# Kernel optimization log

Hardware: AMD Instinct MI355X
Metric: run time of the kernel (lower is better)

The kernel has to match this reference:

```python
import jax, jax.numpy as jnp
import numpy as np

EMBED = 1024
HEADS = 16
HEAD_DIM = EMBED // HEADS
N, L = 8, 1024


def setup_inputs() -> dict:
    key = jax.random.key(0)
    ks = jax.random.split(key, 12)
    s = 1.0 / np.sqrt(EMBED)
    return {
        "values": jax.random.normal(ks[0], (N, L, EMBED), jnp.float32),
        "keys": jax.random.normal(ks[1], (N, L, EMBED), jnp.float32),
        "queries": jax.random.normal(ks[2], (N, L, EMBED), jnp.float32),
        "mask": jax.random.randint(ks[3], (N, 1, L, L), 0, 2, jnp.int32),
        "Wv": jax.random.normal(ks[4], (EMBED, EMBED), jnp.float32) * s,
        "bv": jnp.zeros((EMBED,), jnp.float32),
        "Wk": jax.random.normal(ks[5], (EMBED, EMBED), jnp.float32) * s,
        "bk": jnp.zeros((EMBED,), jnp.float32),
        "Wq": jax.random.normal(ks[6], (EMBED, EMBED), jnp.float32) * s,
        "bq": jnp.zeros((EMBED,), jnp.float32),
        "Wo": jax.random.normal(ks[7], (EMBED, EMBED), jnp.float32) * s,
        "bo": jnp.zeros((EMBED,), jnp.float32),
    }


def reference(values, keys, queries, mask, Wv, bv, Wk, bk, Wq, bq, Wo, bo):
    n, q_len = queries.shape[0], queries.shape[1]
    # Linear projections (torch Linear: x @ W.T + b)
    v = values @ Wv.T + bv
    k = keys @ Wk.T + bk
    q = queries @ Wq.T + bq
    # split heads: [N, L, H, D]
    v = v.reshape(n, -1, HEADS, HEAD_DIM)
    k = k.reshape(n, -1, HEADS, HEAD_DIM)
    q = q.reshape(n, q_len, HEADS, HEAD_DIM)
    # energy: [N, H, Q, K]
    energy = jnp.einsum("nqhd,nkhd->nhqk", q, k)
    energy = jnp.where(mask == 0, jnp.float32(-1e20), energy)
    attention = jax.nn.softmax(energy / jnp.sqrt(jnp.float32(EMBED)), axis=3)
    out = jnp.einsum("nhqk,nkhd->nqhd", attention, v).reshape(n, q_len, EMBED)
    return out @ Wo.T + bo
```

## Files before the change

### kernel.cpp

```cpp
#include <hip/hip_runtime.h>
#include <hip/hip_bf16.h>


typedef __attribute__((ext_vector_type(8))) short short8;
typedef __attribute__((ext_vector_type(8))) __bf16 bf16x8;
typedef __attribute__((ext_vector_type(4))) float f32x4;
typedef __attribute__((ext_vector_type(16))) float f32x16;
typedef __attribute__((ext_vector_type(4))) unsigned short ushort4v;

static __device__ __forceinline__ unsigned short f2bf(float x) {
  union { float f; unsigned u; } v; v.f = x;
  unsigned r = v.u + 0x7FFFu + ((v.u >> 16) & 1u);
  return (unsigned short)(r >> 16);
}

static __device__ __forceinline__ f32x4 mfma16(short8 a, short8 b, f32x4 c) {
  return __builtin_amdgcn_mfma_f32_16x16x32_bf16(
      __builtin_bit_cast(bf16x8, a), __builtin_bit_cast(bf16x8, b), c, 0, 0, 0);
}
static __device__ __forceinline__ f32x16 mfma32(short8 a, short8 b, f32x16 c) {
  return __builtin_amdgcn_mfma_f32_32x32x16_bf16(
      __builtin_bit_cast(bf16x8, a), __builtin_bit_cast(bf16x8, b), c, 0, 0, 0);
}

static __device__ __forceinline__ void gll16(const unsigned short* g, unsigned short* l) {
  __builtin_amdgcn_global_load_lds(
      (const __attribute__((address_space(1))) unsigned int*)(const void*)g,
      (__attribute__((address_space(3))) unsigned int*)(void*)l, 16, 0, 0);
}

static __device__ __forceinline__ unsigned cvtpk(float lo, float hi) {
  unsigned r;
  asm("v_cvt_pk_bf16_f32 %0, %1, %2" : "=v"(r) : "v"(lo), "v"(hi));
  return r;
}

__global__ __launch_bounds__(256)
void cvt_kernel(const float* __restrict__ in, unsigned short* __restrict__ out, int n8)
{
  int i = blockIdx.x * 256 + threadIdx.x;
  if (i >= n8) return;
  float4 a = ((const float4*)in)[i * 2];
  float4 b = ((const float4*)in)[i * 2 + 1];
  union { short8 v; unsigned short u[8]; } pk;
  pk.u[0] = f2bf(a.x); pk.u[1] = f2bf(a.y); pk.u[2] = f2bf(a.z); pk.u[3] = f2bf(a.w);
  pk.u[4] = f2bf(b.x); pk.u[5] = f2bf(b.y); pk.u[6] = f2bf(b.z); pk.u[7] = f2bf(b.w);
  ((short8*)out)[i] = pk.v;
}

__global__ __launch_bounds__(256)
void maskpack_kernel(const int* __restrict__ m, unsigned long long* __restrict__ M64)
{
  const int lane = threadIdx.x & 63, wid = threadIdx.x >> 6;
  const int wi = blockIdx.x * 4 + wid;
  unsigned long long b = __ballot(m[(size_t)wi * 64 + lane] != 0);
  if (lane == 0) M64[wi] = b;
}

template<int MODE>
__global__ __launch_bounds__(256)
void gemm_kernel(const unsigned short* __restrict__ A, const unsigned short* __restrict__ B,
                 const float* __restrict__ bias, void* __restrict__ outp)
{
  __shared__ alignas(16) unsigned short As[128][32];
  __shared__ alignas(16) unsigned short Bs[128][32];
  const int tid = threadIdx.x, lane = tid & 63, wid = tid >> 6;
  const int l15 = lane & 15, lg = lane >> 4;
  const int bm = blockIdx.x, bn = blockIdx.y;
  const int wr = (wid >> 1) * 64, wc = (wid & 1) * 64;

  f32x4 acc[4][4] = {};
  const int o = wid * 1024 + lane * 16;
  const unsigned short* gA0 = A + (size_t)(bm * 128 + (o >> 6)) * 1024 + ((o & 63) >> 1);
  const unsigned short* gA1 = gA0 + 64 * 1024;
  const unsigned short* gB0 = B + (size_t)(bn * 128 + (o >> 6)) * 1024 + ((o & 63) >> 1);
  const unsigned short* gB1 = gB0 + 64 * 1024;
  unsigned short* lA0 = &As[0][0] + wid * 512;
  unsigned short* lA1 = lA0 + 2048;
  unsigned short* lB0 = &Bs[0][0] + wid * 512;
  unsigned short* lB1 = lB0 + 2048;

  for (int k0 = 0; k0 < 1024; k0 += 32) {
    __syncthreads();
    gll16(gA0 + k0, lA0); gll16(gA1 + k0, lA1);
    gll16(gB0 + k0, lB0); gll16(gB1 + k0, lB1);
    __syncthreads();
    short8 af[4], bf[4];
#pragma unroll
    for (int f = 0; f < 4; ++f) {
      af[f] = *(const short8*)&As[wr + f * 16 + l15][lg * 8];
      bf[f] = *(const short8*)&Bs[wc + f * 16 + l15][lg * 8];
    }
#pragma unroll
    for (int r = 0; r < 4; ++r)
#pragma unroll
      for (int c = 0; c < 4; ++c)
        acc[r][c] = mfma16(af[r], bf[c], acc[r][c]);
  }

#pragma unroll
  for (int r = 0; r < 4; ++r) {
    const int mb = bm * 128 + wr + r * 16 + lg * 4;
#pragma unroll
    for (int c = 0; c < 4; ++c) {
      const int col = bn * 128 + wc + c * 16 + l15;
      const float bv = bias[col];
      if (MODE == 0) {
        unsigned short* O = (unsigned short*)outp;
#pragma unroll
        for (int i = 0; i < 4; ++i)
          O[(size_t)(mb + i) * 1024 + col] = f2bf(acc[r][c][i] + bv);
      } else if (MODE == 1) {
        unsigned short* O = (unsigned short*)outp;
        const int n = mb >> 10, l = mb & 1023, hh = col >> 6, d = col & 63;
        union { ushort4v v; unsigned short u[4]; } pk;
#pragma unroll
        for (int i = 0; i < 4; ++i) pk.u[i] = f2bf(acc[r][c][i] + bv);
        *(ushort4v*)&O[(size_t)((n * 16 + hh) * 64 + d) * 1024 + l] = pk.v;
      } else {
        float* O = (float*)outp;
#pragma unroll
        for (int i = 0; i < 4; ++i)
          O[(size_t)(mb + i) * 1024 + col] = acc[r][c][i] + bv;
      }
    }
  }
}

__global__ __launch_bounds__(256)
void attn_kernel(const unsigned short* __restrict__ Q,
                 const unsigned short* __restrict__ K,
                 const unsigned short* __restrict__ VT,
                 const unsigned long long* __restrict__ M64,
                 unsigned short* __restrict__ AO)
{
  __shared__ alignas(16) unsigned short Ks[2][4096];
  __shared__ alignas(16) unsigned short Vs[2][4096];
  const int tid = threadIdx.x, lane = tid & 63, wid = tid >> 6;
  const int l31 = lane & 31, hi4 = (lane >> 5) * 4;
  const int w = (blockIdx.x & 7) * 128 + (blockIdx.x >> 3);
  const int qt = w & 7, nh = w >> 3, h = nh & 15, n = nh >> 4;
  const int qbase = qt * 128 + wid * 32;

  const int o = wid * 1024 + lane * 16;
  const int srow = o >> 7, sswz = ((o >> 4) & 7) ^ (srow & 7);
  const unsigned short* gK0 = K + (size_t)(n * 1024 + srow) * 1024 + h * 64 + sswz * 8;
  const unsigned short* gK1 = gK0 + 32 * 1024;
  const unsigned short* gV0 = VT + (size_t)((n * 16 + h) * 64 + srow) * 1024 + sswz * 8;
  const unsigned short* gV1 = gV0 + 32 * 1024;
  unsigned short* lK[2] = { &Ks[0][0] + wid * 512, &Ks[1][0] + wid * 512 };
  unsigned short* lV[2] = { &Vs[0][0] + wid * 512, &Vs[1][0] + wid * 512 };

  short8 qf[4];
#pragma unroll
  for (int c = 0; c < 4; ++c)
    qf[c] = *(const short8*)&Q[(size_t)(n * 1024 + qbase + l31) * 1024 + h * 64 + c * 16 + hi4 * 2];

  const unsigned long long* Mq = M64 + (size_t)(n * 1024 + qbase + l31) * 16;
  unsigned long long mw = Mq[0], mwn;

  f32x16 oacc0 = {}, oacc1 = {};
  float m_r = -3.0e38f, l_r = 0.f;
  const float SC = 0.03125f * 1.44269504089f;

  gll16(gK0, lK[0]); gll16(gK1, lK[0] + 2048);
  gll16(gV0, lV[0]); gll16(gV1, lV[0] + 2048);

  int cur = 0;
  for (int t = 0; t < 16; ++t) {
    __syncthreads();
    if (t < 15) {
      const size_t ko = (size_t)(t + 1) * 64 * 1024, vo = (size_t)(t + 1) * 64;
      gll16(gK0 + ko, lK[cur ^ 1]); gll16(gK1 + ko, lK[cur ^ 1] + 2048);
      gll16(gV0 + vo, lV[cur ^ 1]); gll16(gV1 + vo, lV[cur ^ 1] + 2048);
      mwn = Mq[t + 1];
    }
    const unsigned short* Kb = &Ks[cur][0];
    const unsigned short* Vb = &Vs[cur][0];

    f32x16 s0 = {}, s1 = {};
#pragma unroll
    for (int c = 0; c < 4; ++c) {
      const int r0 = l31, r1 = 32 + l31;
      short8 kf0 = *(const short8*)&Kb[r0 * 64 + ((((c << 1) + (hi4 >> 2)) ^ (r0 & 7)) << 3)];
      short8 kf1 = *(const short8*)&Kb[r1 * 64 + ((((c << 1) + (hi4 >> 2)) ^ (r1 & 7)) << 3)];
      s0 = mfma32(kf0, qf[c], s0);
      s1 = mfma32(kf1, qf[c], s1);
    }

    const unsigned mlo = (unsigned)mw, mhigh = (unsigned)(mw >> 32);
    float e0[16], e1[16];
#pragma unroll
    for (int r = 0; r < 16; ++r) {
      const unsigned s = (unsigned)(8 * (r >> 2) + (r & 3) + hi4);
      e0[r] = ((mlo  >> s) & 1u) ? s0[r] * SC : -1.0e30f;
      e1[r] = ((mhigh >> s) & 1u) ? s1[r] * SC : -1.0e30f;
    }

    float rm = fmaxf(e0[0], e1[0]);
#pragma unroll
    for (int r = 1; r < 16; ++r) rm = fmaxf(rm, fmaxf(e0[r], e1[r]));
    rm = fmaxf(rm, __shfl_xor(rm, 32));

    if (!__all(rm <= m_r + 11.0f)) {
      const float mn = fmaxf(m_r, rm);
      const float scv = exp2f(m_r - mn);
      l_r *= scv;
      m_r = mn;
      const int scvi = __builtin_bit_cast(int, scv);
#pragma unroll
      for (int r = 0; r < 16; ++r) {
        const int qrow = 8 * (r >> 2) + (r & 3) + hi4;
        const float sr = __builtin_bit_cast(float, __builtin_amdgcn_ds_bpermute(qrow * 4, scvi));
        oacc0[r] *= sr; oacc1[r] *= sr;
      }
    }

    short8 pa[4];
#pragma unroll
    for (int kt = 0; kt < 2; ++kt) {
      float p[16];
      float lsum = 0.f;
#pragma unroll
      for (int r = 0; r < 16; ++r) {
        p[r] = exp2f((kt ? e1[r] : e0[r]) - m_r);
        lsum += p[r];
      }
      l_r += lsum;
      unsigned u[4][2];
#pragma unroll
      for (int g = 0; g < 4; ++g) {
        u[g][0] = cvtpk(p[4 * g], p[4 * g + 1]);
        u[g][1] = cvtpk(p[4 * g + 2], p[4 * g + 3]);
      }
#pragma unroll
      for (int m = 0; m < 2; ++m) {
        unsigned a0 = u[2 * m][0], b0 = u[2 * m + 1][0];
        unsigned a1 = u[2 * m][1], b1 = u[2 * m + 1][1];
        asm("v_permlane32_swap_b32 %0, %1" : "+v"(a0), "+v"(b0));
        asm("v_permlane32_swap_b32 %0, %1" : "+v"(a1), "+v"(b1));
        union { unsigned uu[4]; short8 v; } pk;
        pk.uu[0] = a0; pk.uu[1] = a1; pk.uu[2] = b0; pk.uu[3] = b1;
        pa[kt * 2 + m] = pk.v;
      }
    }

#pragma unroll
    for (int kt = 0; kt < 4; ++kt) {
      const int r0 = l31, r1 = 32 + l31;
      short8 vf0 = *(const short8*)&Vb[r0 * 64 + ((((kt << 1) + (hi4 >> 2)) ^ (r0 & 7)) << 3)];
      short8 vf1 = *(const short8*)&Vb[r1 * 64 + ((((kt << 1) + (hi4 >> 2)) ^ (r1 & 7)) << 3)];
      oacc0 = mfma32(pa[kt], vf0, oacc0);
      oacc1 = mfma32(pa[kt], vf1, oacc1);
    }

    mw = mwn;
    cur ^= 1;
  }

  const float l_tot = l_r + __shfl_xor(l_r, 32);
  const float inv_l = 1.0f / l_tot;
  const int invi = __builtin_bit_cast(int, inv_l);
#pragma unroll
  for (int r = 0; r < 16; ++r) {
    const int qrow = 8 * (r >> 2) + (r & 3) + hi4;
    const float rl = __builtin_bit_cast(float, __builtin_amdgcn_ds_bpermute(qrow * 4, invi));
    const size_t row = (size_t)(n * 1024 + qbase + qrow) * 1024 + h * 64;
    AO[row + l31]      = f2bf(oacc0[r] * rl);
    AO[row + 32 + l31] = f2bf(oacc1[r] * rl);
  }
}

extern "C" void kernel_launch(void* const* d_in, const int* in_sizes, int n_in,
                              void* d_out, int out_size, void* d_ws, size_t ws_size,
                              hipStream_t stream) {
  (void)in_sizes; (void)n_in; (void)out_size;
  const float* values  = (const float*)d_in[0];
  const float* keys    = (const float*)d_in[1];
  const float* queries = (const float*)d_in[2];
  const int*   mask    = (const int*)d_in[3];
  const float* Wv = (const float*)d_in[4];
  const float* bv = (const float*)d_in[5];
  const float* Wk = (const float*)d_in[6];
  const float* bk = (const float*)d_in[7];
  const float* Wq = (const float*)d_in[8];
  const float* bq = (const float*)d_in[9];
  const float* Wo = (const float*)d_in[10];
  const float* bo = (const float*)d_in[11];

  const size_t MB = 1u << 20;
  char* ws = (char*)d_ws;
  unsigned short* Xb  = (unsigned short*)(ws);
  unsigned short* Qb  = (unsigned short*)(ws + 16 * MB);
  unsigned short* Kb  = (unsigned short*)(ws + 32 * MB);
  unsigned short* VTb = (unsigned short*)(ws + 48 * MB);
  unsigned short* Wb  = (unsigned short*)(ws + 64 * MB);
  unsigned long long* M64 = (unsigned long long*)(ws + 66 * MB);
  unsigned short* Vb  = (unsigned short*)(ws + 67 * MB);
  const bool bigws = ws_size >= 84 * MB;

  const dim3 gG(64, 8), b256(256);
  const int NX8 = 8 * 1024 * 1024 / 8, NW8 = 1024 * 1024 / 8;

  cvt_kernel<<<NX8 / 256, b256, 0, stream>>>(queries, Xb, NX8);
  cvt_kernel<<<NW8 / 256, b256, 0, stream>>>(Wq, Wb, NW8);
  gemm_kernel<0><<<gG, b256, 0, stream>>>(Xb, Wb, bq, (void*)Qb);

  cvt_kernel<<<NX8 / 256, b256, 0, stream>>>(keys, Xb, NX8);
  cvt_kernel<<<NW8 / 256, b256, 0, stream>>>(Wk, Wb, NW8);
  gemm_kernel<0><<<gG, b256, 0, stream>>>(Xb, Wb, bk, (void*)Kb);

  cvt_kernel<<<NX8 / 256, b256, 0, stream>>>(values, Xb, NX8);
  cvt_kernel<<<NW8 / 256, b256, 0, stream>>>(Wv, Wb, NW8);
  if (bigws) {
    gemm_kernel<0><<<gG, b256, 0, stream>>>(Xb, Wb, bv, (void*)Vb);
  }
  gemm_kernel<1><<<gG, b256, 0, stream>>>(Xb, Wb, bv, (void*)VTb);

  maskpack_kernel<<<131072 / 4, b256, 0, stream>>>(mask, M64);

  attn_kernel<<<dim3(1024), b256, 0, stream>>>(Qb, Kb, VTb, M64, Xb );

  cvt_kernel<<<NW8 / 256, b256, 0, stream>>>(Wo, Wb, NW8);
  gemm_kernel<2><<<gG, b256, 0, stream>>>(Xb, Wb, bo, d_out);
}
```

Measured before the change: 263.2 us.

## Apply attention mask after exponentiation and drop the unused V projection GEMM

The softmax no longer builds masked score arrays before the row max. It takes the max over the raw MFMA scores, folds the scale into an FMA inside exp2, and zeroes masked probabilities with a bitwise AND built from the packed mask word. The rescale threshold is rescaled to raw-score units. Separately, the extra row-major V projection GEMM that ran when the workspace was large is removed, since attention only reads the transposed V buffer. A row with every key masked would now give a zero denominator instead of uniform weights.

Measured after the change: 239.4 us. 1.1x faster.

```diff
diff --git a/kernel.cpp b/kernel.cpp
--- a/kernel.cpp
+++ b/kernel.cpp
@@ -188,23 +188,14 @@
       s1 = mfma32(kf1, qf[c], s1);
     }
 
-    const unsigned mlo = (unsigned)mw, mhigh = (unsigned)(mw >> 32);
-    float e0[16], e1[16];
-#pragma unroll
-    for (int r = 0; r < 16; ++r) {
-      const unsigned s = (unsigned)(8 * (r >> 2) + (r & 3) + hi4);
-      e0[r] = ((mlo  >> s) & 1u) ? s0[r] * SC : -1.0e30f;
-      e1[r] = ((mhigh >> s) & 1u) ? s1[r] * SC : -1.0e30f;
-    }
-
-    float rm = fmaxf(e0[0], e1[0]);
-#pragma unroll
-    for (int r = 1; r < 16; ++r) rm = fmaxf(rm, fmaxf(e0[r], e1[r]));
+    float rm = fmaxf(s0[0], s1[0]);
+#pragma unroll
+    for (int r = 1; r < 16; ++r) rm = fmaxf(rm, fmaxf(s0[r], s1[r]));
     rm = fmaxf(rm, __shfl_xor(rm, 32));
 
-    if (!__all(rm <= m_r + 11.0f)) {
+    if (!__all(rm <= m_r + 160.0f)) {
       const float mn = fmaxf(m_r, rm);
-      const float scv = exp2f(m_r - mn);
+      const float scv = exp2f((m_r - mn) * SC);
       l_r *= scv;
       m_r = mn;
       const int scvi = __builtin_bit_cast(int, scv);
@@ -215,15 +206,23 @@
         oacc0[r] *= sr; oacc1[r] *= sr;
       }
     }
-
+    const float nms = -m_r * SC;
+
+    const unsigned wlo = (unsigned)mw >> hi4;
+    const unsigned whi = (unsigned)(mw >> 32) >> hi4;
     short8 pa[4];
 #pragma unroll
     for (int kt = 0; kt < 2; ++kt) {
+      const unsigned wsh = kt ? whi : wlo;
       float p[16];
       float lsum = 0.f;
 #pragma unroll
       for (int r = 0; r < 16; ++r) {
-        p[r] = exp2f((kt ? e1[r] : e0[r]) - m_r);
+        const float sv = kt ? s1[r] : s0[r];
+        const float pe = exp2f(fmaf(sv, SC, nms));
+        const int pos = 8 * (r >> 2) + (r & 3);
+        const int msk = ((int)(wsh << (31 - pos))) >> 31;
+        p[r] = __builtin_bit_cast(float, __builtin_bit_cast(int, pe) & msk);
         lsum += p[r];
       }
       l_r += lsum;
@@ -274,7 +273,7 @@
 extern "C" void kernel_launch(void* const* d_in, const int* in_sizes, int n_in,
                               void* d_out, int out_size, void* d_ws, size_t ws_size,
                               hipStream_t stream) {
-  (void)in_sizes; (void)n_in; (void)out_size;
+  (void)in_sizes; (void)n_in; (void)out_size; (void)ws_size;
   const float* values  = (const float*)d_in[0];
   const float* keys    = (const float*)d_in[1];
   const float* queries = (const float*)d_in[2];
@@ -296,8 +295,6 @@
   unsigned short* VTb = (unsigned short*)(ws + 48 * MB);
   unsigned short* Wb  = (unsigned short*)(ws + 64 * MB);
   unsigned long long* M64 = (unsigned long long*)(ws + 66 * MB);
-  unsigned short* Vb  = (unsigned short*)(ws + 67 * MB);
-  const bool bigws = ws_size >= 84 * MB;
 
   const dim3 gG(64, 8), b256(256);
   const int NX8 = 8 * 1024 * 1024 / 8, NW8 = 1024 * 1024 / 8;
@@ -312,9 +309,6 @@
 
   cvt_kernel<<<NX8 / 256, b256, 0, stream>>>(values, Xb, NX8);
   cvt_kernel<<<NW8 / 256, b256, 0, stream>>>(Wv, Wb, NW8);
-  if (bigws) {
-    gemm_kernel<0><<<gG, b256, 0, stream>>>(Xb, Wb, bv, (void*)Vb);
-  }
   gemm_kernel<1><<<gG, b256, 0, stream>>>(Xb, Wb, bv, (void*)VTb);
 
   maskpack_kernel<<<131072 / 4, b256, 0, stream>>>(mask, M64);
```
